# Performance work log

Hardware: AMD Instinct MI355X
Metric: run time of the kernel (lower is better)

## Reference

```python
import jax, jax.numpy as jnp
import numpy as np


def make_dictionary(T, Drr, Dtheta):
    # rows i=0..T-1; (-Drr)**i == (-1)**i * Drr**i for integer i
    idx = jnp.arange(T, dtype=Drr.dtype)[:, None]                      # [T,1]
    sign = jnp.where(jnp.arange(T)[:, None] % 2 == 0, 1.0, -1.0).astype(Drr.dtype)
    ri = Drr[None, :] ** idx                                           # [T,N]
    c = jnp.cos(idx * Dtheta[None, :])
    s = jnp.sin(idx * Dtheta[None, :])
    dic = jnp.concatenate(
        [jnp.ones((T, 1), Drr.dtype), ri * c, sign * ri * c, ri * s, sign * ri * s],
        axis=1,
    )                                                                  # [T, 1+4N]
    G = jnp.linalg.norm(dic, axis=0)
    G = jnp.where(G == 0, jnp.sqrt(jnp.asarray(T, dic.dtype)), G)
    return dic / G


def softshrink(x, lam):
    return jnp.sign(x) * jnp.maximum(jnp.abs(x) - lam, 0.0)


def fista(D, Y, lambd=0.1, max_iter=100, tol=1e-4):
    # D: [T,K], Y: [B,T,F]
    K = D.shape[1]
    DtD = D.T @ D                                                      # [K,K]
    linv = 1.0 / jnp.linalg.norm(DtD)  # torch.norm(DtD, 2) == Frobenius norm
    DtY = jnp.einsum('tk,btf->bkf', D, Y) * linv                       # [B,K,F]
    A = jnp.eye(K, dtype=D.dtype) - DtD * linv
    lam = lambd * linv
    x0 = jnp.zeros_like(DtY)

    def cond(s):
        _, _, _, it, done = s
        return (it < max_iter) & jnp.logical_not(done)

    def body(s):
        x_old, y_old, t, it, done = s
        x_new = softshrink(jnp.einsum('kj,bjf->bkf', A, y_old) + DtY, lam)
        t_new = (1.0 + jnp.sqrt(1.0 + 4.0 * t * t)) / 2.0
        tt = (t - 1.0) / t_new
        y_new = (1.0 + tt) * x_new - tt * x_old
        conv = jnp.linalg.norm((x_new - x_old).ravel()) / K < tol
        return (x_new, y_new, jnp.where(conv, t, t_new), it + 1, conv)

    s0 = (x0, x0, jnp.asarray(1.0, D.dtype), jnp.asarray(0, jnp.int32),
          jnp.asarray(False))
    x, _, _, _, _ = jax.lax.while_loop(cond, body, s0)
    return x


def setup_inputs() -> dict:
    key = jax.random.key(0)
    k1, k2, k3 = jax.random.split(key, 3)
    return {
        'x': jax.random.normal(k1, (2, 36, 20480), jnp.float32),
        'Drr': jax.random.uniform(k2, (40,), dtype=jnp.float32),
        'Dtheta': jax.random.uniform(k3, (40,), dtype=jnp.float32),
        'T': 36,
    }


def reference(x, Drr, Dtheta, T):
    D = make_dictionary(T, Drr, Dtheta)
    return fista(D, x, lambd=0.1, max_iter=100)
```

## Files before the change

### kernel.cpp

```cpp
#include <hip/hip_runtime.h>
#include <math.h>

typedef _Float16 half8 __attribute__((ext_vector_type(8)));
typedef _Float16 half4 __attribute__((ext_vector_type(4)));
typedef float    f32x4 __attribute__((ext_vector_type(4)));

#define T_DIM 36
#define N_AT 40
#define K_REAL 161
#define MT 11
#define KSM 5
#define KS2 2
#define B_DIM 2
#define F_DIM 20480
#define CB 32
#define NTHREADS 256
#define SETUP_T 512
#define MAXIT 100
#define YST 72
#define FSLAB (KSM * 512)

#define WS_AFRAG_OFF 64
#define AFRAG_BYTES (MT * KSM * 2 * 1024)
#define WS_DFRAG_OFF (WS_AFRAG_OFF + AFRAG_BYTES)
#define DFRAG_BYTES (MT * KS2 * 2 * 1024)
#define WS_A160_OFF (WS_DFRAG_OFF + DFRAG_BYTES)

#define MFMA16(a, b, c) __builtin_amdgcn_mfma_f32_16x16x32_f16((a), (b), (c), 0, 0, 0)

__global__ void setup_kernel(const float* __restrict__ Drr,
                             const float* __restrict__ Dtheta,
                             float* __restrict__ ws) {
    __shared__ float Dl[K_REAL][T_DIM];
    __shared__ float red[SETUP_T];
    __shared__ float s_linv;
    int tid = threadIdx.x;

    if (tid < K_REAL) {
        float col[T_DIM];
        if (tid == 0) {
            for (int i = 0; i < T_DIM; ++i) col[i] = 1.0f;
        } else {
            int q = (tid - 1) / N_AT, n = (tid - 1) % N_AT;
            float r = Drr[n], th = Dtheta[n];
            float ri = 1.0f;
            for (int i = 0; i < T_DIM; ++i) {
                float c = cosf((float)i * th), s = sinf((float)i * th);
                float sign = (i & 1) ? -1.0f : 1.0f;
                float v;
                if (q == 0)      v = ri * c;
                else if (q == 1) v = sign * ri * c;
                else if (q == 2) v = ri * s;
                else             v = sign * ri * s;
                col[i] = v;
                ri *= r;
            }
        }
        float ss = 0.0f;
        for (int i = 0; i < T_DIM; ++i) ss += col[i] * col[i];
        float G = sqrtf(ss);
        float Ginv = (G == 0.0f) ? (1.0f / sqrtf((float)T_DIM)) : (1.0f / G);
        for (int i = 0; i < T_DIM; ++i) Dl[tid][i] = col[i] * Ginv;
    }
    __syncthreads();

    float local = 0.0f;
    for (int p = tid; p < K_REAL * K_REAL; p += SETUP_T) {
        int a = p / K_REAL, b = p % K_REAL;
        float dot = 0.0f;
        for (int i = 0; i < T_DIM; ++i) dot += Dl[a][i] * Dl[b][i];
        local += dot * dot;
    }
    red[tid] = local;
    __syncthreads();
    if (tid == 0) {
        float tot = 0.0f;
        for (int i = 0; i < SETUP_T; ++i) tot += red[i];
        float linv = 1.0f / sqrtf(tot);
        s_linv = linv;
        ws[0] = linv;
        ws[1] = 0.1f * linv;
    }
    __syncthreads();
    float linv = s_linv;

    _Float16* wsA = (_Float16*)((char*)ws + WS_AFRAG_OFF);
    int lane = tid >> 3, e = tid & 7;
    int fm = lane & 15, fq = lane >> 4;
    for (int p = 0; p < MT * KSM; ++p) {
        int Mt = p / KSM, ks = p % KSM;
        int m = Mt * 16 + fm;
        int k = ks * 32 + fq * 8 + e;
        float v = 0.0f;
        if (m < K_REAL) {
            float dot = 0.0f;
            for (int t = 0; t < T_DIM; ++t) dot += Dl[m][t] * Dl[k][t];
            v = ((m == k) ? 1.0f : 0.0f) - linv * dot;
        }
        _Float16 h = (_Float16)v;
        _Float16 l = (_Float16)(v - (float)h);
        int base = (p * 2) * 512 + lane * 8 + e;
        wsA[base]       = h;
        wsA[base + 512] = l;
    }

    _Float16* wsD = (_Float16*)((char*)ws + WS_DFRAG_OFF);
    for (int p = 0; p < MT * KS2; ++p) {
        int Mt = p / KS2, ks2 = p % KS2;
        int kr = Mt * 16 + fm;
        int t  = ks2 * 32 + fq * 8 + e;
        float v = (kr < K_REAL && t < T_DIM) ? linv * Dl[kr][t] : 0.0f;
        _Float16 h = (_Float16)v;
        _Float16 l = (_Float16)(v - (float)h);
        int base = (p * 2) * 512 + lane * 8 + e;
        wsD[base]       = h;
        wsD[base + 512] = l;
    }

    float* wsC = (float*)((char*)ws + WS_A160_OFF);
    if (tid < MT * 16) {
        int m = tid;
        float v = 0.0f;
        if (m < K_REAL) {
            float dot = 0.0f;
            for (int t = 0; t < T_DIM; ++t) dot += Dl[m][t] * Dl[160][t];
            v = ((m == 160) ? 1.0f : 0.0f) - linv * dot;
        }
        wsC[m] = v;
    }
}

template <int G>
__device__ __forceinline__ void sweep_g(f32x4 (&acc)[3], const f32x4 (&dty)[3],
                                        const half8 (&Af)[3][KSM][2],
                                        const float (&a160)[3][4],
                                        const _Float16 (*YF)[2][FSLAB],
                                        const _Float16 (*Y160s)[16],
                                        int lane, int cl, int mlc) {
    const half8* fh = (const half8*)&YF[G][0][0];
    const half8* fl = (const half8*)&YF[G][1][0];
    #pragma unroll
    for (int ks = 0; ks < KSM; ++ks) {
        half8 yh = fh[ks * 64 + lane];
        half8 yl = fl[ks * 64 + lane];
        #pragma unroll
        for (int ml = 0; ml < 3; ++ml) {
            if (ml < mlc) {
                f32x4 c0 = (ks == 0) ? dty[ml] : acc[ml];
                c0 = MFMA16(Af[ml][ks][0], yh, c0);
                c0 = MFMA16(Af[ml][ks][0], yl, c0);
                acc[ml] = MFMA16(Af[ml][ks][1], yh, c0);
            }
        }
    }
    float y160 = (float)Y160s[2 * G + 0][cl] + (float)Y160s[2 * G + 1][cl];
    #pragma unroll
    for (int ml = 0; ml < 3; ++ml)
        if (ml < mlc)
            #pragma unroll
            for (int r = 0; r < 4; ++r)
                acc[ml][r] += a160[ml][r] * y160;
}

template <int G>
__device__ __forceinline__ void epi_g(const f32x4 (&acc)[3], float (&xold)[3][4],
                                      _Float16 (*YF)[2][FSLAB],
                                      _Float16 (*Y160s)[16],
                                      float lam, float tt,
                                      int cl, int quad, int mg, int mlc) {
    char* ph = (char*)&YF[G][0][0];
    char* pl = (char*)&YF[G][1][0];
    #pragma unroll
    for (int ml = 0; ml < 3; ++ml) {
        if (ml < mlc) {
            const int t = mg * 3 + ml;
            if (t < 10) {
                half4 hv, lv;
                #pragma unroll
                for (int r = 0; r < 4; ++r) {
                    float v  = acc[ml][r];
                    float xn = v - fminf(fmaxf(v, -lam), lam);
                    float yn = xn + tt * (xn - xold[ml][r]);
                    xold[ml][r] = xn;
                    _Float16 h = (_Float16)yn;
                    hv[r] = h;
                    lv[r] = (_Float16)(yn - (float)h);
                }
                int off = t * 512 + ((quad >> 1) << 8) + (cl << 4) + ((quad & 1) << 3);
                *(half4*)(ph + off) = hv;
                *(half4*)(pl + off) = lv;
            } else {
                if (quad == 0) {
                    float v  = acc[ml][0];
                    float xn = v - fminf(fmaxf(v, -lam), lam);
                    float yn = xn + tt * (xn - xold[ml][0]);
                    xold[ml][0] = xn;
                    _Float16 h = (_Float16)yn;
                    Y160s[2 * G + 0][cl] = h;
                    Y160s[2 * G + 1][cl] = (_Float16)(yn - (float)h);
                }
            }
        }
    }
}

__global__ void __launch_bounds__(NTHREADS, 2)
fista_mfma(const float* __restrict__ Y, const float* __restrict__ ws,
           float* __restrict__ out) {
    __shared__ __align__(16) _Float16 YF[2][2][FSLAB];
    __shared__ __align__(16) _Float16 Y160s[4][16];

    const float lam = ((const float*)ws)[1];
    const half8* Afp = (const half8*)((const char*)ws + WS_AFRAG_OFF);
    const half8* Dfp = (const half8*)((const char*)ws + WS_DFRAG_OFF);
    const float* A160 = (const float*)((const char*)ws + WS_A160_OFF);

    const int tid  = threadIdx.x;
    const int lane = tid & 63;
    const int mg   = __builtin_amdgcn_readfirstlane(tid >> 6);
    const int mlc  = (mg == 3) ? 2 : 3;
    const int quad = lane >> 4;
    const int cl   = lane & 15;

    const int blk = blockIdx.x;
    const int b   = blk / (F_DIM / CB);
    const int f0  = (blk % (F_DIM / CB)) * CB;

    _Float16* sh = &YF[0][0][0];
    _Float16* sl = &YF[0][1][0];
    const float* Yb = Y + (size_t)b * T_DIM * F_DIM + f0;
    for (int idx = tid; idx < 64 * CB; idx += NTHREADS) {
        int t = idx / CB, c = idx % CB;
        float v = (t < T_DIM) ? Yb[(size_t)t * F_DIM + c] : 0.0f;
        _Float16 h = (_Float16)v;
        _Float16 l = (_Float16)(v - (float)h);
        sh[c * YST + t] = h;
        sl[c * YST + t] = l;
    }
    __syncthreads();

    f32x4 dty[2][3];
    #pragma unroll
    for (int g = 0; g < 2; ++g)
        #pragma unroll
        for (int ml = 0; ml < 3; ++ml) dty[g][ml] = f32x4{0.f, 0.f, 0.f, 0.f};
    #pragma unroll
    for (int ks2 = 0; ks2 < KS2; ++ks2) {
        #pragma unroll
        for (int g = 0; g < 2; ++g) {
            half8 yh = *(const half8*)&sh[(g * 16 + cl) * YST + ks2 * 32 + quad * 8];
            half8 yl = *(const half8*)&sl[(g * 16 + cl) * YST + ks2 * 32 + quad * 8];
            #pragma unroll
            for (int ml = 0; ml < 3; ++ml) {
                if (ml < mlc) {
                    int Mt = mg * 3 + ml;
                    half8 dh = Dfp[((Mt * KS2 + ks2) * 2 + 0) * 64 + lane];
                    half8 dl = Dfp[((Mt * KS2 + ks2) * 2 + 1) * 64 + lane];
                    dty[g][ml] = MFMA16(dh, yh, dty[g][ml]);
                    dty[g][ml] = MFMA16(dh, yl, dty[g][ml]);
                    dty[g][ml] = MFMA16(dl, yh, dty[g][ml]);
                }
            }
        }
    }
    __syncthreads();

    half8 Af[3][KSM][2];
    float a160[3][4];
    #pragma unroll
    for (int ml = 0; ml < 3; ++ml) {
        if (ml < mlc) {
            #pragma unroll
            for (int ks = 0; ks < KSM; ++ks)
                #pragma unroll
                for (int term = 0; term < 2; ++term)
                    Af[ml][ks][term] =
                        Afp[(((mg * 3 + ml) * KSM + ks) * 2 + term) * 64 + lane];
            #pragma unroll
            for (int r = 0; r < 4; ++r)
                a160[ml][r] = A160[(mg * 3 + ml) * 16 + quad * 4 + r];
        }
    }

    float xoldA[3][4], xoldB[3][4];
    #pragma unroll
    for (int ml = 0; ml < 3; ++ml)
        #pragma unroll
        for (int r = 0; r < 4; ++r) { xoldA[ml][r] = 0.0f; xoldB[ml][r] = 0.0f; }

    f32x4 accA[3], accB[3];
    #pragma unroll
    for (int ml = 0; ml < 3; ++ml) { accA[ml] = dty[0][ml]; accB[ml] = dty[1][ml]; }

    float tm = 1.61803398875f;
    float tt_prev = 0.0f;

    epi_g<0>(accA, xoldA, YF, Y160s, lam, tt_prev, cl, quad, mg, mlc);
    __syncthreads();

    for (int s = 2; s <= MAXIT; ++s) {
        float tn = 0.5f * (1.0f + sqrtf(1.0f + 4.0f * tm * tm));
        float tt_cur = (tm - 1.0f) / tn;
        tm = tn;

        sweep_g<0>(accA, dty[0], Af, a160, YF, Y160s, lane, cl, mlc);
        epi_g<1>(accB, xoldB, YF, Y160s, lam, tt_prev, cl, quad, mg, mlc);
        __syncthreads();

        sweep_g<1>(accB, dty[1], Af, a160, YF, Y160s, lane, cl, mlc);
        epi_g<0>(accA, xoldA, YF, Y160s, lam, tt_cur, cl, quad, mg, mlc);
        __syncthreads();

        tt_prev = tt_cur;
    }
    epi_g<1>(accB, xoldB, YF, Y160s, lam, tt_prev, cl, quad, mg, mlc);

    #pragma unroll
    for (int g = 0; g < 2; ++g) {
        float* ob = out + (size_t)b * K_REAL * F_DIM + f0 + g * 16 + cl;
        #pragma unroll
        for (int ml = 0; ml < 3; ++ml)
            if (ml < mlc)
                #pragma unroll
                for (int r = 0; r < 4; ++r) {
                    int k = (mg * 3 + ml) * 16 + quad * 4 + r;
                    float xv = g ? xoldB[ml][r] : xoldA[ml][r];
                    if (k < K_REAL) ob[(size_t)k * F_DIM] = xv;
                }
    }
}

extern "C" void kernel_launch(void* const* d_in, const int* in_sizes, int n_in,
                              void* d_out, int out_size, void* d_ws, size_t ws_size,
                              hipStream_t stream) {
    const float* x      = (const float*)d_in[0];
    const float* Drr    = (const float*)d_in[1];
    const float* Dtheta = (const float*)d_in[2];
    float* out = (float*)d_out;
    float* ws  = (float*)d_ws;

    hipLaunchKernelGGL(setup_kernel, dim3(1), dim3(SETUP_T), 0, stream,
                       Drr, Dtheta, ws);
    hipLaunchKernelGGL(fista_mfma, dim3((B_DIM * F_DIM) / CB), dim3(NTHREADS),
                       0, stream, x, ws, out);
}
```

Measured before the change: 707.1 us.

## Split M-tiles across six waves per block and stage A160 in LDS

Raises the block from 4 to 6 waves so each wave owns 2 row tiles of the iteration matrix instead of 3. This shortens the serial MFMA chain per wave and adds wavefronts to hide latency. The A160 column now sits in shared memory instead of registers, which frees VGPRs toward the 3-blocks-per-CU launch bound. The epilogue switches to packed round-toward-zero fp16 conversions, which slightly changes the hi/lo split rounding, and the extra waves add barrier cost.

```diff
diff --git a/kernel.cpp b/kernel.cpp
--- a/kernel.cpp
+++ b/kernel.cpp
@@ -3,6 +3,7 @@
 
 typedef _Float16 half8 __attribute__((ext_vector_type(8)));
 typedef _Float16 half4 __attribute__((ext_vector_type(4)));
+typedef __fp16   fp16x2 __attribute__((ext_vector_type(2)));
 typedef float    f32x4 __attribute__((ext_vector_type(4)));
 
 #define T_DIM 36
@@ -14,7 +15,7 @@
 #define B_DIM 2
 #define F_DIM 20480
 #define CB 32
-#define NTHREADS 256
+#define NTHREADS 384
 #define SETUP_T 512
 #define MAXIT 100
 #define YST 72
@@ -131,20 +132,25 @@
 }
 
 template <int G>
-__device__ __forceinline__ void sweep_g(f32x4 (&acc)[3], const f32x4 (&dty)[3],
-                                        const half8 (&Af)[3][KSM][2],
-                                        const float (&a160)[3][4],
+__device__ __forceinline__ void sweep_g(f32x4 (&acc)[2], const f32x4 (&dty)[2],
+                                        const half8 (&Af)[2][KSM][2],
                                         const _Float16 (*YF)[2][FSLAB],
                                         const _Float16 (*Y160s)[16],
-                                        int lane, int cl, int mlc) {
+                                        const float* __restrict__ A160L,
+                                        int lane, int cl, int quad, int wv, int mlc) {
     const half8* fh = (const half8*)&YF[G][0][0];
     const half8* fl = (const half8*)&YF[G][1][0];
+    f32x4 a160v[2];
+    #pragma unroll
+    for (int ml = 0; ml < 2; ++ml)
+        if (ml < mlc)
+            a160v[ml] = *(const f32x4*)&A160L[(wv * 2 + ml) * 16 + quad * 4];
     #pragma unroll
     for (int ks = 0; ks < KSM; ++ks) {
         half8 yh = fh[ks * 64 + lane];
         half8 yl = fl[ks * 64 + lane];
         #pragma unroll
-        for (int ml = 0; ml < 3; ++ml) {
+        for (int ml = 0; ml < 2; ++ml) {
             if (ml < mlc) {
                 f32x4 c0 = (ks == 0) ? dty[ml] : acc[ml];
                 c0 = MFMA16(Af[ml][ks][0], yh, c0);
@@ -155,37 +161,47 @@
     }
     float y160 = (float)Y160s[2 * G + 0][cl] + (float)Y160s[2 * G + 1][cl];
     #pragma unroll
-    for (int ml = 0; ml < 3; ++ml)
+    for (int ml = 0; ml < 2; ++ml)
         if (ml < mlc)
             #pragma unroll
             for (int r = 0; r < 4; ++r)
-                acc[ml][r] += a160[ml][r] * y160;
+                acc[ml][r] += a160v[ml][r] * y160;
 }
 
 template <int G>
-__device__ __forceinline__ void epi_g(const f32x4 (&acc)[3], float (&xold)[3][4],
+__device__ __forceinline__ void epi_g(const f32x4 (&acc)[2], float (&xold)[2][4],
                                       _Float16 (*YF)[2][FSLAB],
                                       _Float16 (*Y160s)[16],
                                       float lam, float tt,
-                                      int cl, int quad, int mg, int mlc) {
+                                      int cl, int quad, int wv, int mlc) {
     char* ph = (char*)&YF[G][0][0];
     char* pl = (char*)&YF[G][1][0];
     #pragma unroll
-    for (int ml = 0; ml < 3; ++ml) {
+    for (int ml = 0; ml < 2; ++ml) {
         if (ml < mlc) {
-            const int t = mg * 3 + ml;
+            const int t = wv * 2 + ml;
             if (t < 10) {
-                half4 hv, lv;
+                float yn[4];
                 #pragma unroll
                 for (int r = 0; r < 4; ++r) {
                     float v  = acc[ml][r];
                     float xn = v - fminf(fmaxf(v, -lam), lam);
-                    float yn = xn + tt * (xn - xold[ml][r]);
+                    yn[r] = xn + tt * (xn - xold[ml][r]);
                     xold[ml][r] = xn;
-                    _Float16 h = (_Float16)yn;
-                    hv[r] = h;
-                    lv[r] = (_Float16)(yn - (float)h);
                 }
+                fp16x2 h01 = __builtin_amdgcn_cvt_pkrtz(yn[0], yn[1]);
+                fp16x2 h23 = __builtin_amdgcn_cvt_pkrtz(yn[2], yn[3]);
+                float l0 = yn[0] - (float)h01[0];
+                float l1 = yn[1] - (float)h01[1];
+                float l2 = yn[2] - (float)h23[0];
+                float l3 = yn[3] - (float)h23[1];
+                fp16x2 l01 = __builtin_amdgcn_cvt_pkrtz(l0, l1);
+                fp16x2 l23 = __builtin_amdgcn_cvt_pkrtz(l2, l3);
+                half4 hv, lv;
+                hv[0] = (_Float16)h01[0]; hv[1] = (_Float16)h01[1];
+                hv[2] = (_Float16)h23[0]; hv[3] = (_Float16)h23[1];
+                lv[0] = (_Float16)l01[0]; lv[1] = (_Float16)l01[1];
+                lv[2] = (_Float16)l23[0]; lv[3] = (_Float16)l23[1];
                 int off = t * 512 + ((quad >> 1) << 8) + (cl << 4) + ((quad & 1) << 3);
                 *(half4*)(ph + off) = hv;
                 *(half4*)(pl + off) = lv;
@@ -204,11 +220,12 @@
     }
 }
 
-__global__ void __launch_bounds__(NTHREADS, 2)
+__global__ void __launch_bounds__(NTHREADS, 3)
 fista_mfma(const float* __restrict__ Y, const float* __restrict__ ws,
            float* __restrict__ out) {
     __shared__ __align__(16) _Float16 YF[2][2][FSLAB];
     __shared__ __align__(16) _Float16 Y160s[4][16];
+    __shared__ __align__(16) float A160L[MT * 16];
 
     const float lam = ((const float*)ws)[1];
     const half8* Afp = (const half8*)((const char*)ws + WS_AFRAG_OFF);
@@ -217,8 +234,8 @@
 
     const int tid  = threadIdx.x;
     const int lane = tid & 63;
-    const int mg   = __builtin_amdgcn_readfirstlane(tid >> 6);
-    const int mlc  = (mg == 3) ? 2 : 3;
+    const int wv   = __builtin_amdgcn_readfirstlane(tid >> 6);
+    const int mlc  = (wv == 5) ? 1 : 2;
     const int quad = lane >> 4;
     const int cl   = lane & 15;
 
@@ -237,13 +254,14 @@
         sh[c * YST + t] = h;
         sl[c * YST + t] = l;
     }
-    __syncthreads();
-
-    f32x4 dty[2][3];
+    if (tid < MT * 16) A160L[tid] = A160[tid];
+    __syncthreads();
+
+    f32x4 dty[2][2];
     #pragma unroll
     for (int g = 0; g < 2; ++g)
         #pragma unroll
-        for (int ml = 0; ml < 3; ++ml) dty[g][ml] = f32x4{0.f, 0.f, 0.f, 0.f};
+        for (int ml = 0; ml < 2; ++ml) dty[g][ml] = f32x4{0.f, 0.f, 0.f, 0.f};
     #pragma unroll
     for (int ks2 = 0; ks2 < KS2; ++ks2) {
         #pragma unroll
@@ -251,9 +269,9 @@
             half8 yh = *(const half8*)&sh[(g * 16 + cl) * YST + ks2 * 32 + quad * 8];
             half8 yl = *(const half8*)&sl[(g * 16 + cl) * YST + ks2 * 32 + quad * 8];
             #pragma unroll
-            for (int ml = 0; ml < 3; ++ml) {
+            for (int ml = 0; ml < 2; ++ml) {
                 if (ml < mlc) {
-                    int Mt = mg * 3 + ml;
+                    int Mt = wv * 2 + ml;
                     half8 dh = Dfp[((Mt * KS2 + ks2) * 2 + 0) * 64 + lane];
                     half8 dl = Dfp[((Mt * KS2 + ks2) * 2 + 1) * 64 + lane];
                     dty[g][ml] = MFMA16(dh, yh, dty[g][ml]);
@@ -265,37 +283,31 @@
     }
     __syncthreads();
 
-    half8 Af[3][KSM][2];
-    float a160[3][4];
-    #pragma unroll
-    for (int ml = 0; ml < 3; ++ml) {
-        if (ml < mlc) {
+    half8 Af[2][KSM][2];
+    #pragma unroll
+    for (int ml = 0; ml < 2; ++ml)
+        if (ml < mlc)
             #pragma unroll
             for (int ks = 0; ks < KSM; ++ks)
                 #pragma unroll
                 for (int term = 0; term < 2; ++term)
                     Af[ml][ks][term] =
-                        Afp[(((mg * 3 + ml) * KSM + ks) * 2 + term) * 64 + lane];
-            #pragma unroll
-            for (int r = 0; r < 4; ++r)
-                a160[ml][r] = A160[(mg * 3 + ml) * 16 + quad * 4 + r];
-        }
-    }
-
-    float xoldA[3][4], xoldB[3][4];
-    #pragma unroll
-    for (int ml = 0; ml < 3; ++ml)
+                        Afp[(((wv * 2 + ml) * KSM + ks) * 2 + term) * 64 + lane];
+
+    float xoldA[2][4], xoldB[2][4];
+    #pragma unroll
+    for (int ml = 0; ml < 2; ++ml)
         #pragma unroll
         for (int r = 0; r < 4; ++r) { xoldA[ml][r] = 0.0f; xoldB[ml][r] = 0.0f; }
 
-    f32x4 accA[3], accB[3];
-    #pragma unroll
-    for (int ml = 0; ml < 3; ++ml) { accA[ml] = dty[0][ml]; accB[ml] = dty[1][ml]; }
+    f32x4 accA[2], accB[2];
+    #pragma unroll
+    for (int ml = 0; ml < 2; ++ml) { accA[ml] = dty[0][ml]; accB[ml] = dty[1][ml]; }
 
     float tm = 1.61803398875f;
     float tt_prev = 0.0f;
 
-    epi_g<0>(accA, xoldA, YF, Y160s, lam, tt_prev, cl, quad, mg, mlc);
+    epi_g<0>(accA, xoldA, YF, Y160s, lam, tt_prev, cl, quad, wv, mlc);
     __syncthreads();
 
     for (int s = 2; s <= MAXIT; ++s) {
@@ -303,27 +315,27 @@
         float tt_cur = (tm - 1.0f) / tn;
         tm = tn;
 
-        sweep_g<0>(accA, dty[0], Af, a160, YF, Y160s, lane, cl, mlc);
-        epi_g<1>(accB, xoldB, YF, Y160s, lam, tt_prev, cl, quad, mg, mlc);
+        sweep_g<0>(accA, dty[0], Af, YF, Y160s, A160L, lane, cl, quad, wv, mlc);
+        epi_g<1>(accB, xoldB, YF, Y160s, lam, tt_prev, cl, quad, wv, mlc);
         __syncthreads();
 
-        sweep_g<1>(accB, dty[1], Af, a160, YF, Y160s, lane, cl, mlc);
-        epi_g<0>(accA, xoldA, YF, Y160s, lam, tt_cur, cl, quad, mg, mlc);
+        sweep_g<1>(accB, dty[1], Af, YF, Y160s, A160L, lane, cl, quad, wv, mlc);
+        epi_g<0>(accA, xoldA, YF, Y160s, lam, tt_cur, cl, quad, wv, mlc);
         __syncthreads();
 
         tt_prev = tt_cur;
     }
-    epi_g<1>(accB, xoldB, YF, Y160s, lam, tt_prev, cl, quad, mg, mlc);
+    epi_g<1>(accB, xoldB, YF, Y160s, lam, tt_prev, cl, quad, wv, mlc);
 
     #pragma unroll
     for (int g = 0; g < 2; ++g) {
         float* ob = out + (size_t)b * K_REAL * F_DIM + f0 + g * 16 + cl;
         #pragma unroll
-        for (int ml = 0; ml < 3; ++ml)
+        for (int ml = 0; ml < 2; ++ml)
             if (ml < mlc)
                 #pragma unroll
                 for (int r = 0; r < 4; ++r) {
-                    int k = (mg * 3 + ml) * 16 + quad * 4 + r;
+                    int k = (wv * 2 + ml) * 16 + quad * 4 + r;
                     float xv = g ? xoldB[ml][r] : xoldA[ml][r];
                     if (k < K_REAL) ob[(size_t)k * F_DIM] = xv;
                 }
```

Result: slower. 1.021 ms (+44.4%).
